# Kernel tuning notes

Hardware: AMD Instinct MI355X
Metric: run time of the kernel (lower is better)

## Reference

```python
import jax, jax.numpy as jnp
import numpy as np
from jax import lax

# Sign table S[m, j, k]: output blade m = sum_{j,k} S[m,j,k] * conv_j(a_k),
# transcribed directly from apply_ga3. Blade order: 0,1,2,3,12,23,13,123.
_TERMS = [
    [(0,0,1),(1,1,1),(2,2,1),(3,3,1),(4,4,-1),(5,5,-1),(6,6,-1),(7,7,-1)],
    [(1,0,1),(0,1,1),(2,4,1),(4,2,-1),(3,6,1),(6,3,-1),(5,7,-1),(7,5,-1)],
    [(2,0,1),(0,2,1),(1,4,-1),(4,1,1),(3,5,1),(5,3,-1),(6,7,1),(7,6,1)],
    [(3,0,1),(0,3,1),(1,6,-1),(6,1,1),(2,5,-1),(5,2,1),(4,7,-1),(7,4,-1)],
    [(4,0,1),(0,4,1),(2,1,1),(1,2,-1),(3,7,1),(7,3,1),(6,5,1),(5,6,-1)],
    [(5,0,1),(0,5,1),(3,2,1),(2,3,-1),(1,7,1),(7,1,1),(4,6,1),(6,4,-1)],
    [(6,0,1),(0,6,1),(3,1,1),(1,3,-1),(2,7,-1),(7,2,-1),(5,4,1),(4,5,-1)],
    [(7,0,1),(0,7,1),(5,1,1),(1,5,1),(6,2,-1),(2,6,-1),(4,3,1),(3,4,1)],
]
_S = np.zeros((8, 8, 8), dtype=np.float32)
for m, terms in enumerate(_TERMS):
    for j, k, s in terms:
        _S[m, j, k] = s
SIGNS = jnp.asarray(_S)


def setup_inputs() -> dict:
    key = jax.random.key(0)
    k1, k2, k3 = jax.random.split(key, 3)
    B, Cin, Cout, H = 8, 16, 16, 128
    x = jax.random.normal(k1, (B, 8 * Cin, H, H), dtype=jnp.float32)
    # Kaiming-uniform-ish small init like nn.Conv2d default scale
    fan_in = Cin * 9
    bound = 1.0 / np.sqrt(fan_in)
    W = jax.random.uniform(k2, (8, Cout, Cin, 3, 3), dtype=jnp.float32,
                           minval=-bound, maxval=bound)
    b = jax.random.uniform(k3, (8, Cout), dtype=jnp.float32,
                           minval=-bound, maxval=bound)
    return {"x": x, "W": W, "b": b}


def reference(x, W, b):
    # x: [B, 8*Cin, H, W] (channel c -> blade c%8, group c//8)
    # W: [8, Cout, Cin, kh, kw]; b: [8, Cout]
    B, C, H, Wd = x.shape
    nW, Cout, Cin, kh, kw = W.shape
    # Split interleaved blades: a[k] = x[:, k::8]  -> [8, B, Cin, H, W]
    a = x.reshape(B, Cin, 8, H, Wd).transpose(2, 0, 1, 3, 4)
    a = a.reshape(8 * B, Cin, H, Wd)                     # fold blade k into batch
    W_all = W.reshape(8 * Cout, Cin, kh, kw)             # all 8 convs at once
    pad = [(1, 1), (1, 1)]
    f = lax.conv_general_dilated(a, W_all, window_strides=(1, 1), padding=pad)
    f = f + b.reshape(1, 8 * Cout, 1, 1)
    Ho, Wo = f.shape[-2:]
    f = f.reshape(8, B, 8, Cout, Ho, Wo)                 # [k, B, j, Cout, H', W']
    # out[m] = sum_{j,k} S[m,j,k] * conv_j(a_k)
    out = jnp.einsum('mjk,kbjchw->bcmhw', SIGNS, f)
    # make_ga3: interleave blades back into channels
    return out.reshape(B, Cout * 8, Ho, Wo)
```

## Files before the change

### kernel.cpp

```cpp
#include <hip/hip_runtime.h>
#include <stdint.h>
#include <stddef.h>


typedef __attribute__((ext_vector_type(8))) short short8;
typedef __attribute__((ext_vector_type(4))) float f32x4;

__device__ __constant__ int c_J[64] = {
  0,1,2,3,4,5,6,7,
  1,0,4,6,2,7,3,5,
  2,4,0,5,1,3,7,6,
  3,6,5,0,7,2,1,4,
  4,2,1,7,0,6,5,3,
  5,7,3,2,6,0,4,1,
  6,3,7,1,5,4,0,2,
  7,5,6,4,3,1,2,0
};
__device__ __constant__ float c_Sg[64] = {
  1,1,1,1,-1,-1,-1,-1,
  1,1,-1,-1,1,-1,1,-1,
  1,1,1,-1,-1,1,1,1,
  1,1,1,1,-1,-1,-1,-1,
  1,1,-1,1,1,1,-1,1,
  1,1,1,-1,-1,1,1,1,
  1,1,-1,-1,1,-1,1,-1,
  1,1,-1,1,1,1,-1,1
};

__device__ inline unsigned short f2bf(float f) {
  unsigned int u = __float_as_uint(f);
  u += 0x7FFFu + ((u >> 16) & 1u);
  return (unsigned short)(u >> 16);
}

__global__ __launch_bounds__(256) void xpose_kernel(const float* __restrict__ x,
                                                    unsigned short* __restrict__ xt) {
  __shared__ unsigned short t[128 * 129];
  const int h   = blockIdx.x;
  const int b   = blockIdx.y;
  const int tid = threadIdx.x;
  #pragma unroll
  for (int i = 0; i < 16; ++i) {
    int idx = tid + i * 256;
    int ic = idx >> 5, wq = idx & 31;
    const float4 v = *(const float4*)(x + ((size_t)(b * 128 + ic) * 128 + h) * 128 + 4 * wq);
    unsigned short* d = t + ic * 129 + 4 * wq;
    d[0] = f2bf(v.x); d[1] = f2bf(v.y); d[2] = f2bf(v.z); d[3] = f2bf(v.w);
  }
  if (tid < 128) {
    int c = tid >> 6, u = tid & 63;
    *(unsigned int*)(xt + ((size_t)(b * 130 + h + 1) * 130 + c * 129) * 128 + 2 * u) = 0u;
  }
  if (h == 0 || h == 127) {
    int row = (h == 0) ? 0 : 129;
    for (int i = 0; i < 33; ++i) {
      int idx = tid + i * 256;
      if (idx < 8320) {
        int w = idx >> 6, u = idx & 63;
        *(unsigned int*)(xt + ((size_t)(b * 130 + row) * 130 + w) * 128 + 2 * u) = 0u;
      }
    }
  }
  __syncthreads();
  #pragma unroll
  for (int i = 0; i < 16; ++i) {
    int idx = tid + i * 256;
    int w = idx >> 5, p4 = idx & 31;
    unsigned int s0 = t[(4 * p4 + 0) * 129 + w];
    unsigned int s1 = t[(4 * p4 + 1) * 129 + w];
    unsigned int s2 = t[(4 * p4 + 2) * 129 + w];
    unsigned int s3 = t[(4 * p4 + 3) * 129 + w];
    uint2 o; o.x = s0 | (s1 << 16); o.y = s2 | (s3 << 16);
    *(uint2*)(xt + ((size_t)(b * 130 + h + 1) * 130 + (w + 1)) * 128 + 4 * p4) = o;
  }
}

__global__ __launch_bounds__(256) void prep_kernel(const float* __restrict__ W,
                                                   const float* __restrict__ bias,
                                                   unsigned short* __restrict__ vt,
                                                   float* __restrict__ beff) {
  int gid = blockIdx.x * 256 + threadIdx.x;
  int t   = gid >> 14;
  int rem = gid & 16383;
  int oc  = rem >> 7;
  int ic  = rem & 127;
  int m = oc & 7, cout = oc >> 3;
  int k = ic & 7, cin = ic >> 3;
  int j = c_J[m * 8 + k];
  float s = c_Sg[m * 8 + k];
  float val = s * W[((j * 16 + cout) * 16 + cin) * 9 + t];
  int ks = ic >> 5, quad = (ic >> 3) & 3, e = ic & 7;
  int ocb = oc >> 4, l15 = oc & 15;
  vt[(size_t)((t * 4 + ks) * 8 + ocb) * 512 + (quad * 16 + l15) * 8 + e] = f2bf(val);
  if (gid < 128) {
    int m2 = gid & 7, cout2 = gid >> 3;
    float acc = 0.f;
    #pragma unroll
    for (int kk = 0; kk < 8; ++kk)
      acc += c_Sg[m2 * 8 + kk] * bias[c_J[m2 * 8 + kk] * 16 + cout2];
    beff[gid] = acc;
  }
}

__global__ __launch_bounds__(256) void conv_kernel(const unsigned short* __restrict__ xt,
                                                   const unsigned short* __restrict__ vt,
                                                   const float* __restrict__ beff,
                                                   float* __restrict__ out) {
  __shared__ __align__(16) unsigned short lds_x[10 * 18 * 128];
  const int tid  = threadIdx.x;
  const int bx   = blockIdx.x;
  const int by   = blockIdx.y;
  const int b    = blockIdx.z;
  const int lane = tid & 63;
  const int wave = tid >> 6;
  const int wm   = wave >> 1;
  const int wn   = wave & 1;
  const int l15  = lane & 15;
  const int quad = lane >> 4;

  {
    const unsigned short* xb = xt + ((size_t)(b * 130 + by * 8) * 130 + bx * 16) * 128;
    #pragma unroll
    for (int i = 0; i < 11; ++i) {
      int c  = tid + i * 256;
      int hh = c / 288;
      int r  = c - hh * 288;
      uint4 v = *((const uint4*)(xb + (size_t)hh * (130 * 128)) + r);
      ((uint4*)lds_x)[c ^ ((c >> 4) & 7)] = v;
    }
    if (tid < 64) {
      int c  = tid + 2816;
      int hh = c / 288;
      int r  = c - hh * 288;
      uint4 v = *((const uint4*)(xb + (size_t)hh * (130 * 128)) + r);
      ((uint4*)lds_x)[c ^ ((c >> 4) & 7)] = v;
    }
  }
  __syncthreads();

  f32x4 acc[4][4];
  #pragma unroll
  for (int mi = 0; mi < 4; ++mi)
    #pragma unroll
    for (int ni = 0; ni < 4; ++ni)
      acc[mi][ni] = f32x4{0.f, 0.f, 0.f, 0.f};

  const unsigned short* vtw = vt + (size_t)(wn * 4) * 512 + (size_t)lane * 8;

  #pragma unroll
  for (int t = 0; t < 9; ++t) {
    const int dh = t / 3, dw = t % 3;
    int rowb[4];
    #pragma unroll
    for (int mi = 0; mi < 4; ++mi)
      rowb[mi] = (wm * 4 + mi + dh) * 18 + l15 + dw;
    #pragma unroll
    for (int ks = 0; ks < 4; ++ks) {
      short8 bb[4];
      #pragma unroll
      for (int ni = 0; ni < 4; ++ni)
        bb[ni] = *(const short8*)(vtw + (size_t)((t * 4 + ks) * 8 + ni) * 512);
      short8 a[4];
      #pragma unroll
      for (int mi = 0; mi < 4; ++mi) {
        int row = rowb[mi];
        int off = row * 256 + ((ks * 64 + quad * 16) ^ ((row & 7) << 4));
        a[mi] = *(const short8*)((const char*)lds_x + off);
      }
      #pragma unroll
      for (int mi = 0; mi < 4; ++mi)
        #pragma unroll
        for (int ni = 0; ni < 4; ++ni)
          acc[mi][ni] = __builtin_amdgcn_mfma_f32_16x16x32_bf16(a[mi], bb[ni], acc[mi][ni], 0, 0, 0);
    }
  }

  const int h0 = by * 8, w0 = bx * 16;
  #pragma unroll
  for (int ni = 0; ni < 4; ++ni) {
    int oc = (wn * 4 + ni) * 16 + l15;
    float bv = beff[oc];
    #pragma unroll
    for (int mi = 0; mi < 4; ++mi) {
      int h = h0 + wm * 4 + mi;
      int w = w0 + quad * 4;
      f32x4 v = acc[mi][ni];
      v[0] += bv; v[1] += bv; v[2] += bv; v[3] += bv;
      *(f32x4*)(out + ((size_t)(b * 128 + oc) * 128 + h) * 128 + w) = v;
    }
  }
}

extern "C" void kernel_launch(void* const* d_in, const int* in_sizes, int n_in,
                              void* d_out, int out_size, void* d_ws, size_t ws_size,
                              hipStream_t stream) {
  (void)in_sizes; (void)n_in; (void)out_size; (void)ws_size;
  const float* x    = (const float*)d_in[0];
  const float* W    = (const float*)d_in[1];
  const float* bias = (const float*)d_in[2];
  float* out = (float*)d_out;

  const size_t XT_BYTES = (size_t)8 * 130 * 130 * 128 * 2;
  const size_t VT_BYTES = (size_t)9 * 4 * 8 * 512 * 2;
  unsigned short* xt = (unsigned short*)d_ws;
  unsigned short* vt = (unsigned short*)((char*)d_ws + XT_BYTES);
  float* beff = (float*)((char*)d_ws + XT_BYTES + VT_BYTES);

  prep_kernel<<<dim3(576), 256, 0, stream>>>(W, bias, vt, beff);
  xpose_kernel<<<dim3(128, 8), 256, 0, stream>>>(x, xt);
  conv_kernel<<<dim3(8, 16, 8), 256, 0, stream>>>(xt, vt, beff, out);
}
```

Before: 153.9 us.

## Double-buffer conv weights in LDS via async global_load_lds

Weights were previously read straight from global memory into registers inside the MFMA loop. They are now staged into a two-slot LDS buffer with global_load_lds DMA, one half-tap (two k-steps) at a time, while the other slot is being consumed. The goal is to hide weight-fetch latency and let the four waves share one weight load. In exchange it adds 32 KB of LDS, which can lower occupancy, and inserts a barrier plus a full vmcnt wait at every half-tap.

```diff
diff --git a/kernel.cpp b/kernel.cpp
--- a/kernel.cpp
+++ b/kernel.cpp
@@ -5,6 +5,10 @@
 
 typedef __attribute__((ext_vector_type(8))) short short8;
 typedef __attribute__((ext_vector_type(4))) float f32x4;
+
+#define GLD_LDS16(gsrc, ldst) __builtin_amdgcn_global_load_lds( \
+    (const __attribute__((address_space(1))) void*)(gsrc),      \
+    (__attribute__((address_space(3))) void*)(ldst), 16, 0, 0)
 
 __device__ __constant__ int c_J[64] = {
   0,1,2,3,4,5,6,7,
@@ -107,6 +111,7 @@
                                                    const float* __restrict__ beff,
                                                    float* __restrict__ out) {
   __shared__ __align__(16) unsigned short lds_x[10 * 18 * 128];
+  __shared__ __align__(16) unsigned short lds_w[2][64 * 128];
   const int tid  = threadIdx.x;
   const int bx   = blockIdx.x;
   const int by   = blockIdx.y;
@@ -118,6 +123,42 @@
   const int l15  = lane & 15;
   const int quad = lane >> 4;
 
+#define STAGE_HALF(DST, SRCOFF)                                         \
+  {                                                                     \
+    const char* s_ = (const char*)vt + (SRCOFF);                        \
+    _Pragma("unroll")                                                   \
+    for (int i_ = 0; i_ < 4; ++i_) {                                    \
+      int c_ = (tid + i_ * 256) * 16;                                   \
+      GLD_LDS16(s_ + c_, (char*)(DST) + c_);                            \
+    }                                                                   \
+  }
+
+#define HALF_COMPUTE(WBUF, KS0)                                         \
+  {                                                                     \
+    _Pragma("unroll")                                                   \
+    for (int kk = 0; kk < 2; ++kk) {                                    \
+      const int ks = (KS0) + kk;                                        \
+      short8 bb[4];                                                     \
+      _Pragma("unroll")                                                 \
+      for (int ni = 0; ni < 4; ++ni)                                    \
+        bb[ni] = *(const short8*)((WBUF) + (kk * 8 + wn * 4 + ni) * 512 + lane * 8); \
+      short8 a[4];                                                      \
+      _Pragma("unroll")                                                 \
+      for (int mi = 0; mi < 4; ++mi) {                                  \
+        int row = rowb[mi];                                             \
+        int off = row * 256 + ((ks * 64 + quad * 16) ^ ((row & 7) << 4)); \
+        a[mi] = *(const short8*)((const char*)lds_x + off);             \
+      }                                                                 \
+      _Pragma("unroll")                                                 \
+      for (int mi = 0; mi < 4; ++mi)                                    \
+        _Pragma("unroll")                                               \
+        for (int ni = 0; ni < 4; ++ni)                                  \
+          acc[mi][ni] = __builtin_amdgcn_mfma_f32_16x16x32_bf16(a[mi], bb[ni], acc[mi][ni], 0, 0, 0); \
+    }                                                                   \
+  }
+
+  STAGE_HALF(lds_w[0], 0);
+
   {
     const unsigned short* xb = xt + ((size_t)(b * 130 + by * 8) * 130 + bx * 16) * 128;
     #pragma unroll
@@ -136,6 +177,7 @@
       ((uint4*)lds_x)[c ^ ((c >> 4) & 7)] = v;
     }
   }
+  asm volatile("s_waitcnt vmcnt(0)" ::: "memory");
   __syncthreads();
 
   f32x4 acc[4][4];
@@ -144,8 +186,6 @@
     #pragma unroll
     for (int ni = 0; ni < 4; ++ni)
       acc[mi][ni] = f32x4{0.f, 0.f, 0.f, 0.f};
-
-  const unsigned short* vtw = vt + (size_t)(wn * 4) * 512 + (size_t)lane * 8;
 
   #pragma unroll
   for (int t = 0; t < 9; ++t) {
@@ -154,24 +194,17 @@
     #pragma unroll
     for (int mi = 0; mi < 4; ++mi)
       rowb[mi] = (wm * 4 + mi + dh) * 18 + l15 + dw;
-    #pragma unroll
-    for (int ks = 0; ks < 4; ++ks) {
-      short8 bb[4];
-      #pragma unroll
-      for (int ni = 0; ni < 4; ++ni)
-        bb[ni] = *(const short8*)(vtw + (size_t)((t * 4 + ks) * 8 + ni) * 512);
-      short8 a[4];
-      #pragma unroll
-      for (int mi = 0; mi < 4; ++mi) {
-        int row = rowb[mi];
-        int off = row * 256 + ((ks * 64 + quad * 16) ^ ((row & 7) << 4));
-        a[mi] = *(const short8*)((const char*)lds_x + off);
-      }
-      #pragma unroll
-      for (int mi = 0; mi < 4; ++mi)
-        #pragma unroll
-        for (int ni = 0; ni < 4; ++ni)
-          acc[mi][ni] = __builtin_amdgcn_mfma_f32_16x16x32_bf16(a[mi], bb[ni], acc[mi][ni], 0, 0, 0);
+
+    STAGE_HALF(lds_w[1], (size_t)t * 32768 + 16384);
+    HALF_COMPUTE(lds_w[0], 0)
+    asm volatile("s_waitcnt vmcnt(0)" ::: "memory");
+    __syncthreads();
+
+    if (t < 8) STAGE_HALF(lds_w[0], (size_t)(t + 1) * 32768);
+    HALF_COMPUTE(lds_w[1], 2)
+    if (t < 8) {
+      asm volatile("s_waitcnt vmcnt(0)" ::: "memory");
+      __syncthreads();
     }
   }
 
@@ -189,6 +222,8 @@
       *(f32x4*)(out + ((size_t)(b * 128 + oc) * 128 + h) * 128 + w) = v;
     }
   }
+#undef STAGE_HALF
+#undef HALF_COMPUTE
 }
 
 extern "C" void kernel_launch(void* const* d_in, const int* in_sizes, int n_in,
```

Result: no change. 152.6 us (-0.8%).
